# Optimization experiments

Hardware: AMD Instinct MI355X
Metric: run time of the kernel (lower is better)

## Reference

```python
import jax, jax.numpy as jnp
import numpy as np

B, S, HID = 1, 4096, 1024
NH, HD = 16, 64            # heads, per-head dim
BS = 256                    # block size
PB = 256                    # position buckets (= max_relative_positions)
EPS = 1e-7


def make_log_bucket_position(rel, num_buckets, max_position):
    sign = jnp.sign(rel)
    max_exact = num_buckets // 2
    in_exact = (rel < max_exact) & (rel > -max_exact)
    abs_pos = jnp.where(in_exact, max_exact - 1, jnp.abs(rel))
    x = jnp.log((max_position - 1) / max_exact)
    xx = jnp.log(abs_pos / max_exact) / x
    log_pos = jnp.ceil(xx * (max_exact - 1)) + max_exact
    return jnp.where(abs_pos <= max_exact, rel, (log_pos * sign).astype(jnp.int32)).astype(jnp.int32)


def split_into_blocks(x, block_size, axis):
    # [..., S, ...] -> [..., S//bs, bs, ...]; S assumed divisible by bs
    shp = x.shape
    new = shp[:axis] + (shp[axis] // block_size, block_size) + shp[axis + 1:]
    return x.reshape(new)


def concat_3_blocks(x, block_axis, seq_axis, pad_value=0):
    # pad one zero block on each side of the block axis, then concat
    # [prev, cur, next] along the within-block seq axis.
    pad = [(0, 0)] * x.ndim
    pad[block_axis] = (1, 1)
    xp = jnp.pad(x, pad, constant_values=pad_value)
    nb = x.shape[block_axis]
    slices = [jax.lax.dynamic_slice_in_dim(xp, i, nb, block_axis) for i in range(3)]
    return jnp.concatenate(slices, axis=seq_axis)


def layer_norm(x, scale, bias):
    mu = jnp.mean(x, axis=-1, keepdims=True)
    var = jnp.mean(jnp.square(x - mu), axis=-1, keepdims=True)
    return (x - mu) * jax.lax.rsqrt(var + EPS) * scale + bias


def setup_inputs() -> dict:
    key = jax.random.key(0)
    ks = jax.random.split(key, 8)
    d = {
        'hidden_states': jax.random.normal(ks[0], (B, S, HID), jnp.float32) * 0.02,
        'rel_pos_embeddings': jax.random.normal(ks[1], (S, HID), jnp.float32) * 0.02,
        'Wq': jax.random.normal(ks[2], (HID, HID), jnp.float32) * 0.01,
        'bq': jnp.zeros((HID,), jnp.float32),
        'Wk': jax.random.normal(ks[3], (HID, HID), jnp.float32) * 0.01,
        'bk': jnp.zeros((HID,), jnp.float32),
        'Wv': jax.random.normal(ks[4], (HID, HID), jnp.float32) * 0.01,
        'bv': jnp.zeros((HID,), jnp.float32),
        'Wo': jax.random.normal(ks[5], (HID, HID), jnp.float32) * 0.01,
        'bo': jnp.zeros((HID,), jnp.float32),
        'ln_scale': jnp.ones((HID,), jnp.float32),
        'ln_bias': jnp.zeros((HID,), jnp.float32),
    }
    return d


def reference(hidden_states, rel_pos_embeddings, Wq, bq, Wk, bk, Wv, bv, Wo, bo, ln_scale, ln_bias):
    b, s, hid = hidden_states.shape

    def heads(x):
        return x.reshape(x.shape[:-1] + (NH, HD))

    # content projections -> [B, nb, bs, h, d]
    q = split_into_blocks(heads(hidden_states @ Wq + bq), BS, axis=1)
    k = split_into_blocks(heads(hidden_states @ Wk + bk), BS, axis=1)
    v = split_into_blocks(heads(hidden_states @ Wv + bv), BS, axis=1)
    k3 = concat_3_blocks(k, block_axis=1, seq_axis=2)   # [B, nb, 3bs, h, d]
    v3 = concat_3_blocks(v, block_axis=1, seq_axis=2)

    c2c = jnp.einsum('bnqhd,bnkhd->bnhqk', q, k3)

    # position projections, stacked over batch (size-1 batch dim broadcasts in einsum)
    pos_q = split_into_blocks(heads(rel_pos_embeddings @ Wq + bq)[None], BS, axis=1)  # [1, nb, bs, h, d]
    pos_k = split_into_blocks(heads(rel_pos_embeddings @ Wk + bk)[None], BS, axis=1)
    pos_k3 = concat_3_blocks(pos_k, block_axis=1, seq_axis=2)                          # [1, nb, 3bs, h, d]

    rel = jnp.arange(BS, dtype=jnp.int32)[:, None] - jnp.arange(3 * BS, dtype=jnp.int32)[None, :]
    rel = make_log_bucket_position(rel, PB, PB)
    idx = jnp.clip(rel + PB, 0, 2 * PB - 1)            # [bs, 3bs]

    c2p = jnp.einsum('bnqhd,bnkhd->bnhqk', q, pos_k3)  # [B, nb, h, bs, 3bs]
    # faithful to the source: axis-less jnp.take gathers from the FLATTENED
    # score tensor -> [bs, 3bs] bias broadcast over (batch, block, head)
    c2p_bias = jnp.take(c2p, idx)

    p2c = jnp.einsum('bnqhd,bnkhd->bnhqk', pos_q, k3)
    p2c_bias = jnp.take(p2c, idx)

    scale = jnp.sqrt(jnp.asarray(HD * 3, hidden_states.dtype))
    attn = (c2c + c2p_bias + p2c_bias) / scale
    probs = jax.nn.softmax(attn, axis=-1)

    ctx = jnp.einsum('bnhqk,bnkhd->bnqhd', probs, v3)  # [B, nb, bs, h, d]
    ctx = ctx.reshape(b, s, hid)
    out = ctx @ Wo + bo
    return layer_norm(out + hidden_states, ln_scale, ln_bias)
```

## Files before the change

### kernel.cpp

```cpp
#include <hip/hip_runtime.h>
#include <stdint.h>

typedef unsigned short u16;
typedef __bf16 bf16_t;
typedef bf16_t v8bf __attribute__((ext_vector_type(8)));
typedef float v4f __attribute__((ext_vector_type(4)));

#define SEQ   4096
#define HIDN  1024
#define NHEAD 16
#define HDIM  64
#define BLK   256
#define NBLK  16

#define GLOAD_LDS16(g, l) __builtin_amdgcn_global_load_lds( \
  (const __attribute__((address_space(1))) unsigned*)(g), \
  (__attribute__((address_space(3))) unsigned*)(l), 16, 0, 0)

__device__ __forceinline__ u16 f2bf(float f){
  union { float f; unsigned u; } v; v.f = f;
  unsigned r = (v.u + 0x7fffu + ((v.u >> 16) & 1u)) >> 16;
  return (u16)r;
}
__device__ __forceinline__ float bf2f(u16 h){
  union { unsigned u; float f; } v; v.u = ((unsigned)h) << 16;
  return v.f;
}

__global__ __launch_bounds__(256) void k_prep(const float* __restrict__ hidden, u16* __restrict__ hb,
    const float* __restrict__ Wq, const float* __restrict__ Wk,
    const float* __restrict__ Wv, const float* __restrict__ Wo, u16* __restrict__ Wt,
    const float* __restrict__ bq, const float* __restrict__ bk, const float* __restrict__ bv,
    float* __restrict__ bcat,
    const float* __restrict__ rpe, float* __restrict__ posk, float* __restrict__ posq0)
{
  __shared__ float t[32][33];
  __shared__ float red[4][64];
  int b = blockIdx.x, tid = threadIdx.x;
  if (b < 4096){
    int w = b >> 10, tile = b & 1023;
    int k0 = (tile & 31) * 32, n0 = (tile >> 5) * 32;
    const float* W = (w == 0) ? Wq : (w == 1) ? Wk : (w == 2) ? Wv : Wo;
    u16* outp = Wt + (size_t)w * 1024 * 1024;
    int x = tid & 31, y = tid >> 5;
    #pragma unroll
    for (int yy = 0; yy < 32; yy += 8) t[y + yy][x] = W[(size_t)(k0 + y + yy) * 1024 + n0 + x];
    __syncthreads();
    #pragma unroll
    for (int yy = 0; yy < 32; yy += 8) outp[(size_t)(n0 + y + yy) * 1024 + k0 + x] = f2bf(t[x][y + yy]);
  } else if (b < 4608){
    int base = (b - 4096) * 8192;
    #pragma unroll
    for (int j = 0; j < 8; j++){
      int i = base + j * 1024 + tid * 4;
      float4 f = *(const float4*)&hidden[i];
      unsigned u0 = (unsigned)f2bf(f.x) | ((unsigned)f2bf(f.y) << 16);
      unsigned u1 = (unsigned)f2bf(f.z) | ((unsigned)f2bf(f.w) << 16);
      uint2 p; p.x = u0; p.y = u1;
      *(uint2*)&hb[i] = p;
    }
  } else if (b == 4608){
    #pragma unroll
    for (int j = 0; j < 12; j++){
      int i = j * 256 + tid;
      const float* src = i < 1024 ? bq : (i < 2048 ? bk : bv);
      bcat[i] = src[i & 1023];
    }
  } else {
    int pb = b - 4609;
    int d = tid & 63, part = tid >> 6;
    const float* W  = (pb < 256) ? Wk : Wq;
    const float* rv = (pb < 256) ? &rpe[(size_t)pb * 1024] : rpe;
    float s = 0.f;
    for (int k = part * 256; k < part * 256 + 256; k++) s += rv[k] * W[(size_t)k * 1024 + d];
    red[part][d] = s;
    __syncthreads();
    if (part == 0){
      s = red[0][d] + red[1][d] + red[2][d] + red[3][d];
      if (pb < 256) posk[pb * 64 + d] = s + bk[d];
      else          posq0[d] = s + bq[d];
    }
  }
}

__global__ __launch_bounds__(256) void k_gemm_qkv(const u16* __restrict__ A, const u16* __restrict__ Bt,
                                                  const float* __restrict__ bias,
                                                  u16* __restrict__ qk, u16* __restrict__ Vt)
{
  __shared__ alignas(16) u16 As[128 * 32];
  __shared__ alignas(16) u16 Bs[128 * 32];
  int tid = threadIdx.x, lane = tid & 63, wid = tid >> 6;
  int wr = wid >> 1, wc = wid & 1;
  int m0 = blockIdx.y * 128, n0 = blockIdx.x * 128;
  const int K = 1024;

  v4f acc[4][4];
  #pragma unroll
  for (int m = 0; m < 4; m++)
    #pragma unroll
    for (int n = 0; n < 4; n++) acc[m][n] = (v4f){0.f, 0.f, 0.f, 0.f};

  int r = lane & 15, g = lane >> 4;
  int ob0 = wid * 2048;

  for (int kt = 0; kt < K; kt += 32){
    #pragma unroll
    for (int t = 0; t < 2; ++t){
      int ob = ob0 + t * 1024;
      int o  = ob + lane * 16;
      int row = o >> 6, col = (o & 63) >> 1;
      GLOAD_LDS16(&A [(size_t)(m0 + row) * K + kt + col], As + (ob >> 1));
      GLOAD_LDS16(&Bt[(size_t)(n0 + row) * K + kt + col], Bs + (ob >> 1));
    }
    __syncthreads();
    v8bf a[4], bb[4];
    #pragma unroll
    for (int m = 0; m < 4; m++) a[m] = *(const v8bf*)&As[(wr * 64 + m * 16 + r) * 32 + g * 8];
    #pragma unroll
    for (int n = 0; n < 4; n++) bb[n] = *(const v8bf*)&Bs[(wc * 64 + n * 16 + r) * 32 + g * 8];
    #pragma unroll
    for (int m = 0; m < 4; m++)
      #pragma unroll
      for (int n = 0; n < 4; n++)
        acc[m][n] = __builtin_amdgcn_mfma_f32_16x16x32_bf16(a[m], bb[n], acc[m][n], 0, 0, 0);
    __syncthreads();
  }

  #pragma unroll
  for (int m = 0; m < 4; m++)
    #pragma unroll
    for (int n = 0; n < 4; n++){
      int col = n0 + wc * 64 + n * 16 + r;
      float bv = bias[col];
      #pragma unroll
      for (int i = 0; i < 4; i++){
        int row = m0 + wr * 64 + m * 16 + g * 4 + i;
        u16 h = f2bf(acc[m][n][i] + bv);
        if (col < 2048) qk[(size_t)row * 2048 + col] = h;
        else            Vt[(size_t)(col - 2048) * 4096 + row] = h;
      }
    }
}

__global__ __launch_bounds__(256) void k_gemm_out(const u16* __restrict__ A, const u16* __restrict__ Bt,
                                                  const float* __restrict__ bias,
                                                  const float* __restrict__ resid, float* __restrict__ Cout)
{
  __shared__ alignas(16) u16 As[128 * 32];
  __shared__ alignas(16) u16 Bs[128 * 32];
  int tid = threadIdx.x, lane = tid & 63, wid = tid >> 6;
  int wr = wid >> 1, wc = wid & 1;
  int m0 = blockIdx.y * 128, n0 = blockIdx.x * 128;
  const int K = 1024;

  v4f acc[4][4];
  #pragma unroll
  for (int m = 0; m < 4; m++)
    #pragma unroll
    for (int n = 0; n < 4; n++) acc[m][n] = (v4f){0.f, 0.f, 0.f, 0.f};

  int r = lane & 15, g = lane >> 4;
  int ob0 = wid * 2048;

  for (int kt = 0; kt < K; kt += 32){
    #pragma unroll
    for (int t = 0; t < 2; ++t){
      int ob = ob0 + t * 1024;
      int o  = ob + lane * 16;
      int row = o >> 6, col = (o & 63) >> 1;
      GLOAD_LDS16(&A [(size_t)(m0 + row) * K + kt + col], As + (ob >> 1));
      GLOAD_LDS16(&Bt[(size_t)(n0 + row) * K + kt + col], Bs + (ob >> 1));
    }
    __syncthreads();
    v8bf a[4], bb[4];
    #pragma unroll
    for (int m = 0; m < 4; m++) a[m] = *(const v8bf*)&As[(wr * 64 + m * 16 + r) * 32 + g * 8];
    #pragma unroll
    for (int n = 0; n < 4; n++) bb[n] = *(const v8bf*)&Bs[(wc * 64 + n * 16 + r) * 32 + g * 8];
    #pragma unroll
    for (int m = 0; m < 4; m++)
      #pragma unroll
      for (int n = 0; n < 4; n++)
        acc[m][n] = __builtin_amdgcn_mfma_f32_16x16x32_bf16(a[m], bb[n], acc[m][n], 0, 0, 0);
    __syncthreads();
  }

  #pragma unroll
  for (int m = 0; m < 4; m++)
    #pragma unroll
    for (int n = 0; n < 4; n++){
      int col = n0 + wc * 64 + n * 16 + r;
      float bv = bias[col];
      #pragma unroll
      for (int i = 0; i < 4; i++){
        int row = m0 + wr * 64 + m * 16 + g * 4 + i;
        Cout[(size_t)row * 1024 + col] = acc[m][n][i] + bv + resid[(size_t)row * 1024 + col];
      }
    }
}

__global__ __launch_bounds__(256) void k_brow(const u16* __restrict__ qk,
                                              const float* __restrict__ posk, const float* __restrict__ posq0,
                                              float* __restrict__ brow)
{
  int b = blockIdx.x, tid = threadIdx.x;
  if (tid < 32) brow[b * 32 + tid] = 0.f;
  int u = b * 32 + (tid >> 3), sub = tid & 7;
  float c2p = 0.f, p2c = 0.f;
  #pragma unroll
  for (int j = 0; j < 8; j++){
    int d = sub * 8 + j;
    c2p += bf2f(qk[d]) * posk[u * 64 + d];
    p2c += posq0[d] * bf2f(qk[(size_t)u * 2048 + 1024 + d]);
  }
  float v = c2p + p2c;
  v += __shfl_xor(v, 1);
  v += __shfl_xor(v, 2);
  v += __shfl_xor(v, 4);
  if (sub == 0) brow[256 + u] = v;
}

__global__ void k_biasd(const float* __restrict__ brow, float* __restrict__ biasd)
{
  int t = blockIdx.x * blockDim.x + threadIdx.x;
  int rel = t - 767;
  int bucket;
  bool in_exact = (rel < 128) && (rel > -128);
  int abs_pos = in_exact ? 127 : (rel < 0 ? -rel : rel);
  if (abs_pos <= 128) bucket = rel;
  else {
    float xx = logf((float)abs_pos * (1.0f / 128.0f)) / logf(255.0f / 128.0f);
    float lp = ceilf(xx * 127.0f) + 128.0f;
    int sgn = (rel > 0) ? 1 : ((rel < 0) ? -1 : 0);
    bucket = (int)lp * sgn;
  }
  int idx = bucket + 256;
  idx = idx < 0 ? 0 : (idx > 511 ? 511 : idx);
  biasd[t] = brow[idx];
}

__global__ __launch_bounds__(256) void k_attn(const u16* __restrict__ qk, const u16* __restrict__ Vt,
                                              const float* __restrict__ biasd, u16* __restrict__ ctxg)
{
  __shared__ alignas(16) u16 Ks[128 * 64];
  __shared__ alignas(16) u16 Vs[64 * 128];
  __shared__ alignas(16) u16 Ps[4 * 16 * 128];
  __shared__ float bias_s[1024];

  int b = blockIdx.x;
  int h = b & 15, tile = b >> 4;
  int n = tile >> 2, qb0 = (tile & 3) * 64;
  int tid = threadIdx.x, lane = tid & 63, w = tid >> 6;
  int q0 = tile * 64;
  int g0 = (n - 1) * 256;
  const float c1 = 0.07216878364870323f * 1.4426950408889634f;
  int r = lane & 15, g = lane >> 4;

  *(float4*)&bias_s[tid * 4] = *(const float4*)&biasd[tid * 4];

  v8bf qfrag[2];
  {
    const u16* src = &qk[(size_t)(q0 + w * 16 + r) * 2048 + h * 64 + g * 8];
    qfrag[0] = *(const v8bf*)&src[0];
    qfrag[1] = *(const v8bf*)&src[32];
  }

  u16* Pw = &Ps[w * 2048];
  float m4[4], l4[4];
  v4f pacc[4];
  #pragma unroll
  for (int i = 0; i < 4; i++){ m4[i] = -3.0e38f; l4[i] = 0.f; pacc[i] = (v4f){0.f,0.f,0.f,0.f}; }

  for (int c = 0; c < 6; ++c){
    int cb = g0 + c * 128;
    bool oob = (cb < 0) || (cb >= SEQ);
    if (!oob){
      #pragma unroll
      for (int t = 0; t < 4; ++t){
        int row = w * 32 + t * 8 + (lane >> 3);
        int p = lane & 7;
        GLOAD_LDS16(&qk[(size_t)(cb + row) * 2048 + 1024 + h * 64 + ((p ^ (row & 7)) * 8)],
                    Ks + (size_t)(w * 32 + t * 8) * 64);
      }
      #pragma unroll
      for (int t = 0; t < 4; ++t){
        int d = w * 16 + t * 4 + (lane >> 4);
        int p = lane & 15;
        GLOAD_LDS16(&Vt[(size_t)(h * 64 + d) * 4096 + cb + ((p ^ (d & 7)) * 8)],
                    Vs + (size_t)(w * 16 + t * 4) * 128);
      }
    }
    __syncthreads();

    v4f sacc[8];
    #pragma unroll
    for (int t = 0; t < 8; t++) sacc[t] = (v4f){0.f,0.f,0.f,0.f};
    if (!oob){
      #pragma unroll
      for (int ks = 0; ks < 2; ++ks){
        #pragma unroll
        for (int t = 0; t < 8; t++){
          int kr = t * 16 + r;
          v8bf bb = *(const v8bf*)&Ks[kr * 64 + (((4 * ks + g) ^ (kr & 7)) * 8)];
          sacc[t] = __builtin_amdgcn_mfma_f32_16x16x32_bf16(qfrag[ks], bb, sacc[t], 0, 0, 0);
        }
      }
    }

    float sv[8][4];
    float cm[4] = {-3.0e38f, -3.0e38f, -3.0e38f, -3.0e38f};
    int ib = qb0 + g * 4 + 767 - r - c * 128;
    #pragma unroll
    for (int t = 0; t < 8; t++){
      #pragma unroll
      for (int i = 0; i < 4; i++){
        float s = (sacc[t][i] + bias_s[ib + i - t * 16]) * c1;
        sv[t][i] = s;
        cm[i] = fmaxf(cm[i], s);
      }
    }
    #pragma unroll
    for (int i = 0; i < 4; i++){
      cm[i] = fmaxf(cm[i], __shfl_xor(cm[i], 1));
      cm[i] = fmaxf(cm[i], __shfl_xor(cm[i], 2));
      cm[i] = fmaxf(cm[i], __shfl_xor(cm[i], 4));
      cm[i] = fmaxf(cm[i], __shfl_xor(cm[i], 8));
    }
    #pragma unroll
    for (int i = 0; i < 4; i++){
      float mn = fmaxf(m4[i], cm[i]);
      float sc = exp2f(m4[i] - mn);
      m4[i] = mn;
      l4[i] *= sc;
      #pragma unroll
      for (int nn = 0; nn < 4; nn++) pacc[nn][i] *= sc;
    }
    #pragma unroll
    for (int t = 0; t < 8; t++){
      #pragma unroll
      for (int i = 0; i < 4; i++){
        float p = exp2f(sv[t][i] - m4[i]);
        l4[i] += p;
        if (!oob){
          int row = g * 4 + i;
          Pw[row * 128 + (((2 * t + (r >> 3)) ^ (row & 7)) * 8) + (r & 7)] = f2bf(p);
        }
      }
    }

    if (!oob){
      #pragma unroll
      for (int ks = 0; ks < 4; ++ks){
        v8bf a = *(const v8bf*)&Pw[r * 128 + (((4 * ks + g) ^ (r & 7)) * 8)];
        #pragma unroll
        for (int nn = 0; nn < 4; nn++){
          int d = nn * 16 + r;
          v8bf bb = *(const v8bf*)&Vs[d * 128 + (((4 * ks + g) ^ (d & 7)) * 8)];
          pacc[nn] = __builtin_amdgcn_mfma_f32_16x16x32_bf16(a, bb, pacc[nn], 0, 0, 0);
        }
      }
    }
    __syncthreads();
  }

  float inv4[4];
  #pragma unroll
  for (int i = 0; i < 4; i++){
    l4[i] += __shfl_xor(l4[i], 1);
    l4[i] += __shfl_xor(l4[i], 2);
    l4[i] += __shfl_xor(l4[i], 4);
    l4[i] += __shfl_xor(l4[i], 8);
    inv4[i] = 1.0f / l4[i];
  }
  #pragma unroll
  for (int nn = 0; nn < 4; nn++){
    int d = nn * 16 + r;
    #pragma unroll
    for (int i = 0; i < 4; i++){
      int qrow = q0 + w * 16 + g * 4 + i;
      ctxg[(size_t)qrow * 1024 + h * 64 + d] = f2bf(pacc[nn][i] * inv4[i]);
    }
  }
}

__global__ __launch_bounds__(256) void k_ln(float* __restrict__ out,
                                            const float* __restrict__ gamma, const float* __restrict__ beta)
{
  __shared__ float red[8];
  int row = blockIdx.x, tid = threadIdx.x;
  int lane = tid & 63, wid = tid >> 6;
  size_t base = (size_t)row * 1024 + tid * 4;
  float4 xv = *(const float4*)&out[base];
  float v0 = xv.x, v1 = xv.y, v2 = xv.z, v3 = xv.w;
  float s = v0 + v1 + v2 + v3;
  float q = v0 * v0 + v1 * v1 + v2 * v2 + v3 * v3;
  #pragma unroll
  for (int o = 32; o; o >>= 1){ s += __shfl_down(s, o); q += __shfl_down(q, o); }
  if (lane == 0){ red[wid] = s; red[4 + wid] = q; }
  __syncthreads();
  float ts = red[0] + red[1] + red[2] + red[3];
  float tq = red[4] + red[5] + red[6] + red[7];
  float mu = ts * (1.0f / 1024.0f);
  float var = tq * (1.0f / 1024.0f) - mu * mu;
  float rstd = rsqrtf(var + 1e-7f);
  int c = tid * 4;
  out[base + 0] = (v0 - mu) * rstd * gamma[c + 0] + beta[c + 0];
  out[base + 1] = (v1 - mu) * rstd * gamma[c + 1] + beta[c + 1];
  out[base + 2] = (v2 - mu) * rstd * gamma[c + 2] + beta[c + 2];
  out[base + 3] = (v3 - mu) * rstd * gamma[c + 3] + beta[c + 3];
}

extern "C" void kernel_launch(void* const* d_in, const int* in_sizes, int n_in,
                              void* d_out, int out_size, void* d_ws, size_t ws_size,
                              hipStream_t stream)
{
  const float* hidden = (const float*)d_in[0];
  const float* rpe    = (const float*)d_in[1];
  const float* Wq = (const float*)d_in[2];
  const float* bq = (const float*)d_in[3];
  const float* Wk = (const float*)d_in[4];
  const float* bk = (const float*)d_in[5];
  const float* Wv = (const float*)d_in[6];
  const float* bv = (const float*)d_in[7];
  const float* Wo = (const float*)d_in[8];
  const float* bo = (const float*)d_in[9];
  const float* lns = (const float*)d_in[10];
  const float* lnb = (const float*)d_in[11];
  float* out = (float*)d_out;

  char* ws = (char*)d_ws;
  size_t off = 0;
  auto alloc = [&](size_t bytes){ void* p = ws + off; off += (bytes + 255) & ~(size_t)255; return p; };
  u16* hb      = (u16*)alloc((size_t)SEQ * HIDN * 2);
  u16* Wt      = (u16*)alloc((size_t)4 * HIDN * HIDN * 2);
  u16* qk      = (u16*)alloc((size_t)SEQ * 2048 * 2);
  u16* Vt      = (u16*)alloc((size_t)HIDN * SEQ * 2);
  u16* ctxb    = (u16*)alloc((size_t)SEQ * HIDN * 2);
  float* bcat  = (float*)alloc(3072 * 4);
  float* poskf = (float*)alloc(256 * 64 * 4);
  float* posq0 = (float*)alloc(64 * 4);
  float* brow  = (float*)alloc(512 * 4);
  float* biasd = (float*)alloc(1024 * 4);
  (void)ws_size; (void)in_sizes; (void)n_in; (void)out_size;

  k_prep<<<4866, 256, 0, stream>>>(hidden, hb, Wq, Wk, Wv, Wo, Wt,
                                   bq, bk, bv, bcat, rpe, poskf, posq0);

  k_gemm_qkv<<<dim3(24, 32), 256, 0, stream>>>(hb, Wt, bcat, qk, Vt);

  k_brow<<<8, 256, 0, stream>>>(qk, poskf, posq0, brow);
  k_biasd<<<4, 256, 0, stream>>>(brow, biasd);

  k_attn<<<64 * NHEAD, 256, 0, stream>>>(qk, Vt, biasd, ctxb);

  k_gemm_out<<<dim3(8, 32), 256, 0, stream>>>(ctxb, Wt + (size_t)3 * HIDN * HIDN, bo, hidden, out);

  k_ln<<<SEQ, 256, 0, stream>>>(out, lns, lnb);
}
```

Before: 151.8 us.

## Fuse bias-row and bias-table kernels into attention; use 128-query, 512-thread blocks

Removes the k_brow and k_biasd launches by computing the 512-entry bias row and the 1024-entry diagonal bias table inside each attention block, with the scale folded in. The attention block grows to 8 waves covering 128 queries, so each K/V chunk loaded into LDS is shared by twice as many queries. The V-transpose store in the QKV GEMM is packed into 8-byte writes. The trade-off is that every one of 512 blocks redundantly runs a 256×64 dot-product prologue, which adds latency before the main loop.

```diff
diff --git a/kernel.cpp b/kernel.cpp
--- a/kernel.cpp
+++ b/kernel.cpp
@@ -132,12 +132,18 @@
     for (int n = 0; n < 4; n++){
       int col = n0 + wc * 64 + n * 16 + r;
       float bv = bias[col];
-      #pragma unroll
-      for (int i = 0; i < 4; i++){
-        int row = m0 + wr * 64 + m * 16 + g * 4 + i;
-        u16 h = f2bf(acc[m][n][i] + bv);
-        if (col < 2048) qk[(size_t)row * 2048 + col] = h;
-        else            Vt[(size_t)(col - 2048) * 4096 + row] = h;
+      if (n0 < 2048){
+        #pragma unroll
+        for (int i = 0; i < 4; i++){
+          int row = m0 + wr * 64 + m * 16 + g * 4 + i;
+          qk[(size_t)row * 2048 + col] = f2bf(acc[m][n][i] + bv);
+        }
+      } else {
+        unsigned lo = (unsigned)f2bf(acc[m][n][0] + bv) | ((unsigned)f2bf(acc[m][n][1] + bv) << 16);
+        unsigned hi = (unsigned)f2bf(acc[m][n][2] + bv) | ((unsigned)f2bf(acc[m][n][3] + bv) << 16);
+        uint2 pk; pk.x = lo; pk.y = hi;
+        int row = m0 + wr * 64 + m * 16 + g * 4;
+        *(uint2*)&Vt[(size_t)(col - 2048) * 4096 + row] = pk;
       }
     }
 }
@@ -199,64 +205,55 @@
     }
 }
 
-__global__ __launch_bounds__(256) void k_brow(const u16* __restrict__ qk,
+__global__ __launch_bounds__(512) void k_attn(const u16* __restrict__ qk, const u16* __restrict__ Vt,
                                               const float* __restrict__ posk, const float* __restrict__ posq0,
-                                              float* __restrict__ brow)
-{
-  int b = blockIdx.x, tid = threadIdx.x;
-  if (tid < 32) brow[b * 32 + tid] = 0.f;
-  int u = b * 32 + (tid >> 3), sub = tid & 7;
-  float c2p = 0.f, p2c = 0.f;
-  #pragma unroll
-  for (int j = 0; j < 8; j++){
-    int d = sub * 8 + j;
-    c2p += bf2f(qk[d]) * posk[u * 64 + d];
-    p2c += posq0[d] * bf2f(qk[(size_t)u * 2048 + 1024 + d]);
-  }
-  float v = c2p + p2c;
-  v += __shfl_xor(v, 1);
-  v += __shfl_xor(v, 2);
-  v += __shfl_xor(v, 4);
-  if (sub == 0) brow[256 + u] = v;
-}
-
-__global__ void k_biasd(const float* __restrict__ brow, float* __restrict__ biasd)
-{
-  int t = blockIdx.x * blockDim.x + threadIdx.x;
-  int rel = t - 767;
-  int bucket;
-  bool in_exact = (rel < 128) && (rel > -128);
-  int abs_pos = in_exact ? 127 : (rel < 0 ? -rel : rel);
-  if (abs_pos <= 128) bucket = rel;
-  else {
-    float xx = logf((float)abs_pos * (1.0f / 128.0f)) / logf(255.0f / 128.0f);
-    float lp = ceilf(xx * 127.0f) + 128.0f;
-    int sgn = (rel > 0) ? 1 : ((rel < 0) ? -1 : 0);
-    bucket = (int)lp * sgn;
-  }
-  int idx = bucket + 256;
-  idx = idx < 0 ? 0 : (idx > 511 ? 511 : idx);
-  biasd[t] = brow[idx];
-}
-
-__global__ __launch_bounds__(256) void k_attn(const u16* __restrict__ qk, const u16* __restrict__ Vt,
-                                              const float* __restrict__ biasd, u16* __restrict__ ctxg)
+                                              u16* __restrict__ ctxg)
 {
   __shared__ alignas(16) u16 Ks[128 * 64];
   __shared__ alignas(16) u16 Vs[64 * 128];
-  __shared__ alignas(16) u16 Ps[4 * 16 * 128];
+  __shared__ alignas(16) u16 Ps[8 * 16 * 128];
   __shared__ float bias_s[1024];
+  __shared__ float brow_s[512];
 
   int b = blockIdx.x;
-  int h = b & 15, tile = b >> 4;
-  int n = tile >> 2, qb0 = (tile & 3) * 64;
+  int h = b & 15, T = b >> 4;
+  int n = T >> 1, qb0 = (T & 1) * 128;
   int tid = threadIdx.x, lane = tid & 63, w = tid >> 6;
-  int q0 = tile * 64;
+  int q0 = T * 128;
   int g0 = (n - 1) * 256;
   const float c1 = 0.07216878364870323f * 1.4426950408889634f;
   int r = lane & 15, g = lane >> 4;
 
-  *(float4*)&bias_s[tid * 4] = *(const float4*)&biasd[tid * 4];
+  if (tid < 256){
+    int u = tid;
+    float c2p = 0.f, p2c = 0.f;
+    for (int d = 0; d < 64; d++){
+      c2p += bf2f(qk[d]) * posk[u * 64 + d];
+      p2c += posq0[d] * bf2f(qk[(size_t)u * 2048 + 1024 + d]);
+    }
+    brow_s[256 + u] = c2p + p2c;
+  } else {
+    brow_s[tid - 256] = 0.f;
+  }
+  __syncthreads();
+  #pragma unroll
+  for (int j = 0; j < 2; j++){
+    int t = tid * 2 + j;
+    int rel = t - 767;
+    int bucket;
+    bool in_exact = (rel < 128) && (rel > -128);
+    int abs_pos = in_exact ? 127 : (rel < 0 ? -rel : rel);
+    if (abs_pos <= 128) bucket = rel;
+    else {
+      float xx = logf((float)abs_pos * (1.0f / 128.0f)) / logf(255.0f / 128.0f);
+      float lp = ceilf(xx * 127.0f) + 128.0f;
+      int sgn = (rel > 0) ? 1 : ((rel < 0) ? -1 : 0);
+      bucket = (int)lp * sgn;
+    }
+    int idx = bucket + 256;
+    idx = idx < 0 ? 0 : (idx > 511 ? 511 : idx);
+    bias_s[t] = brow_s[idx] * c1;
+  }
 
   v8bf qfrag[2];
   {
@@ -271,23 +268,25 @@
   #pragma unroll
   for (int i = 0; i < 4; i++){ m4[i] = -3.0e38f; l4[i] = 0.f; pacc[i] = (v4f){0.f,0.f,0.f,0.f}; }
 
+  __syncthreads();
+
   for (int c = 0; c < 6; ++c){
     int cb = g0 + c * 128;
     bool oob = (cb < 0) || (cb >= SEQ);
     if (!oob){
       #pragma unroll
-      for (int t = 0; t < 4; ++t){
-        int row = w * 32 + t * 8 + (lane >> 3);
+      for (int t = 0; t < 2; ++t){
+        int row = w * 16 + t * 8 + (lane >> 3);
         int p = lane & 7;
         GLOAD_LDS16(&qk[(size_t)(cb + row) * 2048 + 1024 + h * 64 + ((p ^ (row & 7)) * 8)],
-                    Ks + (size_t)(w * 32 + t * 8) * 64);
-      }
-      #pragma unroll
-      for (int t = 0; t < 4; ++t){
-        int d = w * 16 + t * 4 + (lane >> 4);
+                    Ks + (size_t)(w * 16 + t * 8) * 64);
+      }
+      #pragma unroll
+      for (int t = 0; t < 2; ++t){
+        int d = w * 8 + t * 4 + (lane >> 4);
         int p = lane & 15;
         GLOAD_LDS16(&Vt[(size_t)(h * 64 + d) * 4096 + cb + ((p ^ (d & 7)) * 8)],
-                    Vs + (size_t)(w * 16 + t * 4) * 128);
+                    Vs + (size_t)(w * 8 + t * 4) * 128);
       }
     }
     __syncthreads();
@@ -309,12 +308,12 @@
 
     float sv[8][4];
     float cm[4] = {-3.0e38f, -3.0e38f, -3.0e38f, -3.0e38f};
-    int ib = qb0 + g * 4 + 767 - r - c * 128;
+    int ib = qb0 + w * 16 + g * 4 + 767 - r - c * 128;
     #pragma unroll
     for (int t = 0; t < 8; t++){
       #pragma unroll
       for (int i = 0; i < 4; i++){
-        float s = (sacc[t][i] + bias_s[ib + i - t * 16]) * c1;
+        float s = fmaf(sacc[t][i], c1, bias_s[ib + i - t * 16]);
         sv[t][i] = s;
         cm[i] = fmaxf(cm[i], s);
       }
@@ -439,8 +438,6 @@
   float* bcat  = (float*)alloc(3072 * 4);
   float* poskf = (float*)alloc(256 * 64 * 4);
   float* posq0 = (float*)alloc(64 * 4);
-  float* brow  = (float*)alloc(512 * 4);
-  float* biasd = (float*)alloc(1024 * 4);
   (void)ws_size; (void)in_sizes; (void)n_in; (void)out_size;
 
   k_prep<<<4866, 256, 0, stream>>>(hidden, hb, Wq, Wk, Wv, Wo, Wt,
@@ -448,10 +445,7 @@
 
   k_gemm_qkv<<<dim3(24, 32), 256, 0, stream>>>(hb, Wt, bcat, qk, Vt);
 
-  k_brow<<<8, 256, 0, stream>>>(qk, poskf, posq0, brow);
-  k_biasd<<<4, 256, 0, stream>>>(brow, biasd);
-
-  k_attn<<<64 * NHEAD, 256, 0, stream>>>(qk, Vt, biasd, ctxb);
+  k_attn<<<512, 512, 0, stream>>>(qk, Vt, poskf, posq0, ctxb);
 
   k_gemm_out<<<dim3(8, 32), 256, 0, stream>>>(ctxb, Wt + (size_t)3 * HIDN * HIDN, bo, hidden, out);
 
```

Measured after the change: 170.1 us. 1.12x slower.
